# Kernel tuning notes

Measured on AMD Instinct MI355X. Metric: run time of the kernel, lower is better.

The kernel has to match this reference:

```python
import jax, jax.numpy as jnp
import numpy as np

NUM_HEADS = 12
LN_EPS = 1e-5


def _layernorm(x, w, b):
    m = jnp.mean(x, axis=-1, keepdims=True)
    v = jnp.mean(jnp.square(x - m), axis=-1, keepdims=True)
    return (x - m) * jax.lax.rsqrt(v + LN_EPS) * w + b


def setup_inputs() -> dict:
    key = jax.random.key(0)
    ks = jax.random.split(key, 6)
    B, N, C, H = 8, 1024, 768, 3072
    s = 0.02
    return {
        "x": jax.random.normal(ks[0], (B, N, C), jnp.float32),
        "ln1_w": jnp.ones((C,), jnp.float32),
        "ln1_b": jnp.zeros((C,), jnp.float32),
        "qkv_w": jax.random.normal(ks[1], (3 * C, C), jnp.float32) * s,
        "qkv_b": jnp.zeros((3 * C,), jnp.float32),
        "proj_w": jax.random.normal(ks[2], (C, C), jnp.float32) * s,
        "proj_b": jnp.zeros((C,), jnp.float32),
        "ln2_w": jnp.ones((C,), jnp.float32),
        "ln2_b": jnp.zeros((C,), jnp.float32),
        "fc1_w": jax.random.normal(ks[3], (H, C), jnp.float32) * s,
        "fc1_b": jnp.zeros((H,), jnp.float32),
        "fc2_w": jax.random.normal(ks[4], (C, H), jnp.float32) * s,
        "fc2_b": jnp.zeros((C,), jnp.float32),
    }


def reference(x, ln1_w, ln1_b, qkv_w, qkv_b, proj_w, proj_b,
              ln2_w, ln2_b, fc1_w, fc1_b, fc2_w, fc2_b):
    B, N, C = x.shape
    H = NUM_HEADS
    d = C // H
    scale = d ** (-0.5)

    # --- attention on norm1(x) (size=None path, dropout rates are 0) ---
    h = _layernorm(x, ln1_w, ln1_b)
    qkv = h @ qkv_w.T + qkv_b                      # [B,N,3C]
    qkv = qkv.reshape(B, N, 3, H, d).transpose(2, 0, 3, 1, 4)  # [3,B,H,N,d]
    q, k, v = qkv[0], qkv[1], qkv[2]
    attn = jnp.einsum('bhqd,bhkd->bhqk', q, k) * scale
    attn = jax.nn.softmax(attn, axis=-1)
    o = jnp.einsum('bhqk,bhkd->bhqd', attn, v)     # [B,H,N,d]
    o = o.transpose(0, 2, 1, 3).reshape(B, N, C)
    x_attn = o @ proj_w.T + proj_b

    # --- residual + MLP ---
    x = x + x_attn
    h2 = _layernorm(x, ln2_w, ln2_b)
    h2 = jax.nn.gelu(h2 @ fc1_w.T + fc1_b, approximate=False)
    x = x + (h2 @ fc2_w.T + fc2_b)
    return x
```

## Files before the change

### kernel.cpp

```cpp
#include <hip/hip_runtime.h>
#include <cmath>

typedef __bf16 bf16;
typedef __bf16 bf16x8 __attribute__((ext_vector_type(8)));
typedef __bf16 bf16x4 __attribute__((ext_vector_type(4)));
typedef __bf16 bf16x2 __attribute__((ext_vector_type(2)));
typedef float floatx4 __attribute__((ext_vector_type(4)));

#define MFMA16(A, B, C) __builtin_amdgcn_mfma_f32_16x16x32_bf16((A), (B), (C), 0, 0, 0)

#define GLDS16(g, l)                                                   \
  __builtin_amdgcn_global_load_lds(                                    \
      (const __attribute__((address_space(1))) void*)(g),              \
      (__attribute__((address_space(3))) void*)(l), 16, 0, 0)

static __device__ __forceinline__ int pack2(float a, float b) {
  bf16x2 t;
  t[0] = (bf16)a;
  t[1] = (bf16)b;
  return __builtin_bit_cast(int, t);
}

__global__ __launch_bounds__(256) void pre_kernel(
    const float* __restrict__ x, const float* __restrict__ g,
    const float* __restrict__ be, bf16* __restrict__ h1,
    const float* __restrict__ s0, bf16* __restrict__ d0, int n0,
    const float* __restrict__ s1, bf16* __restrict__ d1, int n1,
    const float* __restrict__ s2, bf16* __restrict__ d2, int n2,
    const float* __restrict__ s3, bf16* __restrict__ d3, int n3) {
  int bid = blockIdx.x;
  int t = threadIdx.x;
  if (bid < 8192) {
    const float* xr = x + (size_t)bid * 768;
    float v0 = xr[t], v1 = xr[t + 256], v2 = xr[t + 512];
    float s = v0 + v1 + v2;
    float s2 = v0 * v0 + v1 * v1 + v2 * v2;
#pragma unroll
    for (int o = 1; o < 64; o <<= 1) {
      s += __shfl_xor(s, o, 64);
      s2 += __shfl_xor(s2, o, 64);
    }
    __shared__ float red[8];
    int w = t >> 6, lane = t & 63;
    if (lane == 0) { red[w] = s; red[4 + w] = s2; }
    __syncthreads();
    float ts = red[0] + red[1] + red[2] + red[3];
    float ts2 = red[4] + red[5] + red[6] + red[7];
    float mean = ts * (1.0f / 768.0f);
    float var = ts2 * (1.0f / 768.0f) - mean * mean;
    float rstd = rsqrtf(var + 1e-5f);
    bf16* orow = h1 + (size_t)bid * 768;
    orow[t]       = (bf16)((v0 - mean) * rstd * g[t]       + be[t]);
    orow[t + 256] = (bf16)((v1 - mean) * rstd * g[t + 256] + be[t + 256]);
    orow[t + 512] = (bf16)((v2 - mean) * rstd * g[t + 512] + be[t + 512]);
    return;
  }
  int i = (bid - 8192) * 256 + t;
  const float* s;
  bf16* d;
  if (i < n0) { s = s0 + (size_t)i * 4; d = d0 + (size_t)i * 4; }
  else if ((i -= n0) < n1) { s = s1 + (size_t)i * 4; d = d1 + (size_t)i * 4; }
  else if ((i -= n1) < n2) { s = s2 + (size_t)i * 4; d = d2 + (size_t)i * 4; }
  else if ((i -= n2) < n3) { s = s3 + (size_t)i * 4; d = d3 + (size_t)i * 4; }
  else return;
  bf16x4 v;
  v[0] = (bf16)s[0]; v[1] = (bf16)s[1]; v[2] = (bf16)s[2]; v[3] = (bf16)s[3];
  *(bf16x4*)d = v;
}

__global__ __launch_bounds__(256) void ln_kernel(const float* __restrict__ x,
                                                 const float* __restrict__ g,
                                                 const float* __restrict__ be,
                                                 bf16* __restrict__ out) {
  int row = blockIdx.x;
  int t = threadIdx.x;
  const float* xr = x + (size_t)row * 768;
  float v0 = xr[t], v1 = xr[t + 256], v2 = xr[t + 512];
  float s = v0 + v1 + v2;
  float s2 = v0 * v0 + v1 * v1 + v2 * v2;
#pragma unroll
  for (int o = 1; o < 64; o <<= 1) {
    s += __shfl_xor(s, o, 64);
    s2 += __shfl_xor(s2, o, 64);
  }
  __shared__ float red[8];
  int w = t >> 6, lane = t & 63;
  if (lane == 0) { red[w] = s; red[4 + w] = s2; }
  __syncthreads();
  float ts = red[0] + red[1] + red[2] + red[3];
  float ts2 = red[4] + red[5] + red[6] + red[7];
  float mean = ts * (1.0f / 768.0f);
  float var = ts2 * (1.0f / 768.0f) - mean * mean;
  float rstd = rsqrtf(var + 1e-5f);
  bf16* orow = out + (size_t)row * 768;
  orow[t]       = (bf16)((v0 - mean) * rstd * g[t]       + be[t]);
  orow[t + 256] = (bf16)((v1 - mean) * rstd * g[t + 256] + be[t + 256]);
  orow[t + 512] = (bf16)((v2 - mean) * rstd * g[t + 512] + be[t + 512]);
}

constexpr int EP_BF16 = 0;
constexpr int EP_RES_F32 = 1;
constexpr int EP_GELU_BF16 = 2;

template <int EP, int NJ>
__global__ __launch_bounds__(256, 3) void gemm_bt(
    const bf16* __restrict__ A, const bf16* __restrict__ Bw,
    const float* __restrict__ bias, const float* __restrict__ resid,
    void* __restrict__ outp, int M, int N, int K) {
  __shared__ alignas(16) bf16 Asl[128 * 64];
  __shared__ alignas(16) bf16 Bsl[NJ * 32 * 64];
  int tid = threadIdx.x;
  int lane = tid & 63, w = tid >> 6;
  int wm = w >> 1, wn = w & 1;
  int q16 = lane & 15, quad = lane >> 4;
  int fid = blockIdx.x + gridDim.x * blockIdx.y;
  int nb = gridDim.x;
  int s = fid >> 3;
  int m0 = ((fid & 7) * (gridDim.y >> 3) + s / nb) * 128;
  int n0 = (s % nb) * (NJ * 32);

  floatx4 acc[4][NJ];
#pragma unroll
  for (int i = 0; i < 4; i++)
#pragma unroll
    for (int j = 0; j < NJ; j++) acc[i][j] = (floatx4){0.f, 0.f, 0.f, 0.f};

  int rIn = lane >> 3;
  int cg = (lane & 7) ^ rIn;
  const bf16* ag[4];
  const bf16* bg[NJ];
#pragma unroll
  for (int q = 0; q < 4; q++)
    ag[q] = A + (size_t)(m0 + (w * 4 + q) * 8 + rIn) * K + cg * 8;
#pragma unroll
  for (int q = 0; q < NJ; q++)
    bg[q] = Bw + (size_t)(n0 + (w * NJ + q) * 8 + rIn) * K + cg * 8;
  bf16* la = &Asl[w * 2048];
  bf16* lb = &Bsl[w * NJ * 512];

  int msel = q16 & 7;
  int offA[2][4], offB[2][NJ];
#pragma unroll
  for (int ks = 0; ks < 2; ks++) {
#pragma unroll
    for (int i = 0; i < 4; i++)
      offA[ks][i] = (wm * 64 + i * 16 + q16) * 64 + (((ks * 4 + quad) ^ msel)) * 8;
#pragma unroll
    for (int j = 0; j < NJ; j++)
      offB[ks][j] = (wn * 16 * NJ + j * 16 + q16) * 64 + (((ks * 4 + quad) ^ msel)) * 8;
  }

  for (int k0 = 0; k0 < K; k0 += 64) {
    __syncthreads();
#pragma unroll
    for (int q = 0; q < 4; q++) {
      GLDS16(ag[q], la + q * 512);
      ag[q] += 64;
    }
#pragma unroll
    for (int q = 0; q < NJ; q++) {
      GLDS16(bg[q], lb + q * 512);
      bg[q] += 64;
    }
    __syncthreads();
#pragma unroll
    for (int ks = 0; ks < 2; ks++) {
      bf16x8 af[4], bfr[NJ];
#pragma unroll
      for (int i = 0; i < 4; i++) af[i] = *(const bf16x8*)&Asl[offA[ks][i]];
#pragma unroll
      for (int j = 0; j < NJ; j++) bfr[j] = *(const bf16x8*)&Bsl[offB[ks][j]];
#pragma unroll
      for (int i = 0; i < 4; i++)
#pragma unroll
        for (int j = 0; j < NJ; j++) acc[i][j] = MFMA16(af[i], bfr[j], acc[i][j]);
    }
  }

#pragma unroll
  for (int i = 0; i < 4; i++) {
#pragma unroll
    for (int j = 0; j < NJ; j++) {
#pragma unroll
      for (int r = 0; r < 4; r++) {
        int m = m0 + wm * 64 + i * 16 + quad * 4 + r;
        int n = n0 + wn * 16 * NJ + j * 16 + q16;
        size_t idx = (size_t)m * N + n;
        float v = acc[i][j][r] + bias[n];
        if constexpr (EP == EP_BF16) {
          ((bf16*)outp)[idx] = (bf16)v;
        } else if constexpr (EP == EP_RES_F32) {
          ((float*)outp)[idx] = v + resid[idx];
        } else {
          float u = v * (2.3022083f + 0.1029443f * v * v);
          float e = __builtin_amdgcn_exp2f(-u);
          float gv = v * __builtin_amdgcn_rcpf(1.0f + e);
          ((bf16*)outp)[idx] = (bf16)gv;
        }
      }
    }
  }
}

__global__ __launch_bounds__(256, 3) void attn_kernel(const bf16* __restrict__ qkv,
                                                      bf16* __restrict__ o) {
  __shared__ alignas(16) bf16 Kl[2][64 * 64];
  __shared__ alignas(16) bf16 Vt[2][64 * 72];
  int tid = threadIdx.x;
  int lane = tid & 63, w = tid >> 6;
  int q16 = lane & 15, quad = lane >> 4;
  int b = blockIdx.y / 12, h = blockIdx.y % 12;
  int qbase = blockIdx.x * 128 + w * 32;
  const int KS = 64 * 2304;

  bf16x8 qf[2][2];
#pragma unroll
  for (int qt = 0; qt < 2; qt++)
#pragma unroll
    for (int c = 0; c < 2; c++)
      qf[qt][c] = *(const bf16x8*)(qkv +
          (size_t)(b * 1024 + qbase + qt * 16 + q16) * 2304 + h * 64 +
          c * 32 + quad * 8);

  int krow = lane >> 3;
  int kchunk = (lane & 7) ^ krow;
  const bf16* kg0 = qkv + (size_t)(b * 1024 + w * 16 + krow) * 2304 + 768 +
                    h * 64 + kchunk * 8;
  const bf16* kg1 = kg0 + 8 * 2304;
  bf16* kdA[2] = {&Kl[0][w * 1024], &Kl[1][w * 1024]};

  int kr = tid >> 2;
  int dbase = (tid & 3) * 16;
  const bf16* vgA = qkv + (size_t)(b * 1024 + kr) * 2304 + 1536 + h * 64 + dbase;
  const bf16* vgB = vgA + 8;
  int vtA[8], vtB[8];
#pragma unroll
  for (int e = 0; e < 8; e++) {
    int dA = dbase + e;
    int dB = dbase + 8 + e;
    vtA[e] = ((dA * 9 + (kr >> 3)) ^ ((dA >> 3) & 7)) * 8 + (kr & 7);
    vtB[e] = ((dB * 9 + (kr >> 3)) ^ ((dB >> 3) & 7)) * 8 + (kr & 7);
  }

  int koff[4][2];
#pragma unroll
  for (int nc = 0; nc < 4; nc++)
#pragma unroll
    for (int ck = 0; ck < 2; ck++) {
      int key = nc * 16 + q16;
      koff[nc][ck] = (key * 8 + ((ck * 4 + quad) ^ (key & 7))) * 8;
    }
  int voff[2][4];
#pragma unroll
  for (int c = 0; c < 2; c++)
#pragma unroll
    for (int dc = 0; dc < 4; dc++) {
      int d = dc * 16 + q16;
      voff[c][dc] = ((d * 9 + (c * 4 + quad)) ^ ((d >> 3) & 7)) * 8;
    }

  int srcLo = q16 + ((quad & 1) << 5);
  int srcHi = srcLo + 16;
  bool loH = quad < 2;

  float lsum[2] = {0.f, 0.f};
  floatx4 oacc[2][4];
#pragma unroll
  for (int qt = 0; qt < 2; qt++)
#pragma unroll
    for (int dc = 0; dc < 4; dc++) oacc[qt][dc] = (floatx4){0.f, 0.f, 0.f, 0.f};

  GLDS16(kg0, kdA[0]);
  GLDS16(kg1, kdA[0] + 512);
  kg0 += KS; kg1 += KS;
  bf16x8 va = *(const bf16x8*)vgA;
  bf16x8 vb = *(const bf16x8*)vgB;
  vgA += KS; vgB += KS;
#pragma unroll
  for (int e = 0; e < 8; e++) Vt[0][vtA[e]] = va[e];
#pragma unroll
  for (int e = 0; e < 8; e++) Vt[0][vtB[e]] = vb[e];
  va = *(const bf16x8*)vgA;
  vb = *(const bf16x8*)vgB;
  vgA += KS; vgB += KS;

  for (int kt = 0; kt < 16; kt++) {
    int cur = kt & 1, nxt = cur ^ 1;
    __syncthreads();
    if (kt < 15) {
      GLDS16(kg0, kdA[nxt]);
      GLDS16(kg1, kdA[nxt] + 512);
      kg0 += KS; kg1 += KS;
#pragma unroll
      for (int e = 0; e < 8; e++) Vt[nxt][vtA[e]] = va[e];
#pragma unroll
      for (int e = 0; e < 8; e++) Vt[nxt][vtB[e]] = vb[e];
      if (kt < 14) {
        va = *(const bf16x8*)vgA;
        vb = *(const bf16x8*)vgB;
        vgA += KS; vgB += KS;
      }
    }

    floatx4 z[2][4];
#pragma unroll
    for (int nc = 0; nc < 4; nc++) {
      bf16x8 k0 = *(const bf16x8*)&Kl[cur][koff[nc][0]];
      bf16x8 k1 = *(const bf16x8*)&Kl[cur][koff[nc][1]];
#pragma unroll
      for (int qt = 0; qt < 2; qt++) {
        floatx4 t = (floatx4){0.f, 0.f, 0.f, 0.f};
        t = MFMA16(k0, qf[qt][0], t);
        t = MFMA16(k1, qf[qt][1], t);
        z[qt][nc] = t;
      }
    }

    bf16x8 vf[2][4];
#pragma unroll
    for (int c = 0; c < 2; c++)
#pragma unroll
      for (int dc = 0; dc < 4; dc++)
        vf[c][dc] = *(const bf16x8*)&Vt[cur][voff[c][dc]];

#pragma unroll
    for (int qt = 0; qt < 2; qt++) {
      float e_[4][4];
#pragma unroll
      for (int nc = 0; nc < 4; nc++)
#pragma unroll
        for (int r = 0; r < 4; r++) {
          e_[nc][r] = __builtin_amdgcn_exp2f(z[qt][nc][r] * 0.18033688011f);
          lsum[qt] += e_[nc][r];
        }
      int P[4][2];
#pragma unroll
      for (int nc = 0; nc < 4; nc++) {
        P[nc][0] = pack2(e_[nc][0], e_[nc][1]);
        P[nc][1] = pack2(e_[nc][2], e_[nc][3]);
      }
      union { int i[4]; bf16x8 v; } pu[2];
#pragma unroll
      for (int c = 0; c < 2; c++) {
        int a0 = __shfl(P[2 * c][0], srcLo, 64), b0 = __shfl(P[2 * c + 1][0], srcLo, 64);
        int a1 = __shfl(P[2 * c][1], srcLo, 64), b1 = __shfl(P[2 * c + 1][1], srcLo, 64);
        int a2 = __shfl(P[2 * c][0], srcHi, 64), b2 = __shfl(P[2 * c + 1][0], srcHi, 64);
        int a3 = __shfl(P[2 * c][1], srcHi, 64), b3 = __shfl(P[2 * c + 1][1], srcHi, 64);
        pu[c].i[0] = loH ? a0 : b0;
        pu[c].i[1] = loH ? a1 : b1;
        pu[c].i[2] = loH ? a2 : b2;
        pu[c].i[3] = loH ? a3 : b3;
      }
#pragma unroll
      for (int dc = 0; dc < 4; dc++) {
        oacc[qt][dc] = MFMA16(pu[0].v, vf[0][dc], oacc[qt][dc]);
        oacc[qt][dc] = MFMA16(pu[1].v, vf[1][dc], oacc[qt][dc]);
      }
    }
  }

#pragma unroll
  for (int qt = 0; qt < 2; qt++) {
    float s = lsum[qt];
    s += __shfl_xor(s, 16, 64);
    s += __shfl_xor(s, 32, 64);
    float inv = 1.0f / s;
    bf16* op = o + (size_t)(b * 1024 + qbase + qt * 16) * 768 + h * 64;
#pragma unroll
    for (int r = 0; r < 4; r++) {
      float invr = __shfl(inv, quad * 4 + r, 64);
#pragma unroll
      for (int dc = 0; dc < 4; dc++)
        op[(size_t)(quad * 4 + r) * 768 + dc * 16 + q16] =
            (bf16)(oacc[qt][dc][r] * invr);
    }
  }
}

extern "C" void kernel_launch(void* const* d_in, const int* in_sizes, int n_in,
                              void* d_out, int out_size, void* d_ws, size_t ws_size,
                              hipStream_t stream) {
  (void)in_sizes; (void)n_in; (void)out_size; (void)ws_size;
  const float* x      = (const float*)d_in[0];
  const float* ln1_w  = (const float*)d_in[1];
  const float* ln1_b  = (const float*)d_in[2];
  const float* qkv_w  = (const float*)d_in[3];
  const float* qkv_b  = (const float*)d_in[4];
  const float* proj_w = (const float*)d_in[5];
  const float* proj_b = (const float*)d_in[6];
  const float* ln2_w  = (const float*)d_in[7];
  const float* ln2_b  = (const float*)d_in[8];
  const float* fc1_w  = (const float*)d_in[9];
  const float* fc1_b  = (const float*)d_in[10];
  const float* fc2_w  = (const float*)d_in[11];
  const float* fc2_b  = (const float*)d_in[12];

  char* ws = (char*)d_ws;
  size_t off = 0;
  auto alloc = [&](size_t bytes) {
    void* p = ws + off;
    off += (bytes + 255) & ~(size_t)255;
    return p;
  };
  bf16* wq  = (bf16*)alloc((size_t)2304 * 768 * 2);
  bf16* wp  = (bf16*)alloc((size_t)768 * 768 * 2);
  bf16* wf1 = (bf16*)alloc((size_t)3072 * 768 * 2);
  bf16* wf2 = (bf16*)alloc((size_t)768 * 3072 * 2);
  bf16* slotA = (bf16*)alloc((size_t)8192 * 768 * 2);
  bf16* slotB = (bf16*)alloc((size_t)8192 * 3072 * 2);
  float* x1 = (float*)alloc((size_t)8192 * 768 * 4);

  bf16* h1 = slotA;
  bf16* qkvb = slotB;
  bf16* ob = slotA;
  bf16* h2 = slotA;
  bf16* hm = slotB;

  pre_kernel<<<8192 + 6912, 256, 0, stream>>>(
      x, ln1_w, ln1_b, h1,
      qkv_w, wq, 2304 * 768 / 4, proj_w, wp, 768 * 768 / 4,
      fc1_w, wf1, 3072 * 768 / 4, fc2_w, wf2, 768 * 3072 / 4);

  gemm_bt<EP_BF16, 4><<<dim3(18, 64), 256, 0, stream>>>(
      h1, wq, qkv_b, nullptr, qkvb, 8192, 2304, 768);
  attn_kernel<<<dim3(8, 96), 256, 0, stream>>>(qkvb, ob);
  gemm_bt<EP_RES_F32, 2><<<dim3(12, 64), 256, 0, stream>>>(
      ob, wp, proj_b, x, x1, 8192, 768, 768);
  ln_kernel<<<8192, 256, 0, stream>>>(x1, ln2_w, ln2_b, h2);
  gemm_bt<EP_GELU_BF16, 4><<<dim3(24, 64), 256, 0, stream>>>(
      h2, wf1, fc1_b, nullptr, hm, 8192, 3072, 768);
  gemm_bt<EP_RES_F32, 2><<<dim3(12, 64), 256, 0, stream>>>(
      hm, wf2, fc2_b, x1, (float*)d_out, 8192, 768, 3072);
}
```

Measured before the change: 343.4 us.

## Template GEMM K-tile depth, vectorize V transpose, reorder attention grid

The GEMM kernel now takes a templated K-tile depth BK with a generalized swizzle. The two N=768 projection GEMMs use BK=128, which halves the number of k-loop iterations and barriers at the cost of more shared memory per block. The attention kernel's V transpose into LDS now does 8-byte loads of four rows and packs them with bit shuffles, replacing 16 scalar bf16 LDS stores per thread. The attention grid is swapped so batch-head varies fastest, which changes block scheduling and L2 locality.

```diff
diff --git a/kernel.cpp b/kernel.cpp
--- a/kernel.cpp
+++ b/kernel.cpp
@@ -6,6 +6,7 @@
 typedef __bf16 bf16x4 __attribute__((ext_vector_type(4)));
 typedef __bf16 bf16x2 __attribute__((ext_vector_type(2)));
 typedef float floatx4 __attribute__((ext_vector_type(4)));
+typedef unsigned int uint;
 
 #define MFMA16(A, B, C) __builtin_amdgcn_mfma_f32_16x16x32_bf16((A), (B), (C), 0, 0, 0)
 
@@ -102,13 +103,18 @@
 constexpr int EP_RES_F32 = 1;
 constexpr int EP_GELU_BF16 = 2;
 
-template <int EP, int NJ>
+template <int EP, int NJ, int BK>
 __global__ __launch_bounds__(256, 3) void gemm_bt(
     const bf16* __restrict__ A, const bf16* __restrict__ Bw,
     const float* __restrict__ bias, const float* __restrict__ resid,
     void* __restrict__ outp, int M, int N, int K) {
-  __shared__ alignas(16) bf16 Asl[128 * 64];
-  __shared__ alignas(16) bf16 Bsl[NJ * 32 * 64];
+  constexpr int GR = BK / 8;
+  constexpr int RC = 64 / GR;
+  constexpr int ACH = 128 / RC / 4;
+  constexpr int BCH = (32 * NJ) / RC / 4;
+  constexpr int NKS = BK / 32;
+  __shared__ alignas(16) bf16 Asl[128 * BK];
+  __shared__ alignas(16) bf16 Bsl[NJ * 32 * BK];
   int tid = threadIdx.x;
   int lane = tid & 63, w = tid >> 6;
   int wm = w >> 1, wn = w & 1;
@@ -125,46 +131,50 @@
 #pragma unroll
     for (int j = 0; j < NJ; j++) acc[i][j] = (floatx4){0.f, 0.f, 0.f, 0.f};
 
-  int rIn = lane >> 3;
-  int cg = (lane & 7) ^ rIn;
-  const bf16* ag[4];
-  const bf16* bg[NJ];
-#pragma unroll
-  for (int q = 0; q < 4; q++)
-    ag[q] = A + (size_t)(m0 + (w * 4 + q) * 8 + rIn) * K + cg * 8;
-#pragma unroll
-  for (int q = 0; q < NJ; q++)
-    bg[q] = Bw + (size_t)(n0 + (w * NJ + q) * 8 + rIn) * K + cg * 8;
-  bf16* la = &Asl[w * 2048];
-  bf16* lb = &Bsl[w * NJ * 512];
-
-  int msel = q16 & 7;
-  int offA[2][4], offB[2][NJ];
-#pragma unroll
-  for (int ks = 0; ks < 2; ks++) {
+  int rIn = lane / GR;
+  int sl = lane & (GR - 1);
+  const bf16* ag[ACH];
+  const bf16* bg[BCH];
+#pragma unroll
+  for (int q = 0; q < ACH; q++) {
+    int row = (w * ACH + q) * RC + rIn;
+    ag[q] = A + (size_t)(m0 + row) * K + (size_t)(sl ^ (row & (GR - 1))) * 8;
+  }
+#pragma unroll
+  for (int q = 0; q < BCH; q++) {
+    int row = (w * BCH + q) * RC + rIn;
+    bg[q] = Bw + (size_t)(n0 + row) * K + (size_t)(sl ^ (row & (GR - 1))) * 8;
+  }
+  bf16* la = &Asl[w * ACH * 512];
+  bf16* lb = &Bsl[w * BCH * 512];
+
+  int swz = q16 & (GR - 1);
+  int offA[NKS][4], offB[NKS][NJ];
+#pragma unroll
+  for (int ks = 0; ks < NKS; ks++) {
 #pragma unroll
     for (int i = 0; i < 4; i++)
-      offA[ks][i] = (wm * 64 + i * 16 + q16) * 64 + (((ks * 4 + quad) ^ msel)) * 8;
+      offA[ks][i] = (wm * 64 + i * 16 + q16) * BK + ((ks * 4 + quad) ^ swz) * 8;
 #pragma unroll
     for (int j = 0; j < NJ; j++)
-      offB[ks][j] = (wn * 16 * NJ + j * 16 + q16) * 64 + (((ks * 4 + quad) ^ msel)) * 8;
-  }
-
-  for (int k0 = 0; k0 < K; k0 += 64) {
+      offB[ks][j] = (wn * 16 * NJ + j * 16 + q16) * BK + ((ks * 4 + quad) ^ swz) * 8;
+  }
+
+  for (int k0 = 0; k0 < K; k0 += BK) {
     __syncthreads();
 #pragma unroll
-    for (int q = 0; q < 4; q++) {
+    for (int q = 0; q < ACH; q++) {
       GLDS16(ag[q], la + q * 512);
-      ag[q] += 64;
-    }
-#pragma unroll
-    for (int q = 0; q < NJ; q++) {
+      ag[q] += BK;
+    }
+#pragma unroll
+    for (int q = 0; q < BCH; q++) {
       GLDS16(bg[q], lb + q * 512);
-      bg[q] += 64;
+      bg[q] += BK;
     }
     __syncthreads();
 #pragma unroll
-    for (int ks = 0; ks < 2; ks++) {
+    for (int ks = 0; ks < NKS; ks++) {
       bf16x8 af[4], bfr[NJ];
 #pragma unroll
       for (int i = 0; i < 4; i++) af[i] = *(const bf16x8*)&Asl[offA[ks][i]];
@@ -209,8 +219,8 @@
   int tid = threadIdx.x;
   int lane = tid & 63, w = tid >> 6;
   int q16 = lane & 15, quad = lane >> 4;
-  int b = blockIdx.y / 12, h = blockIdx.y % 12;
-  int qbase = blockIdx.x * 128 + w * 32;
+  int b = blockIdx.x / 12, h = blockIdx.x % 12;
+  int qbase = blockIdx.y * 128 + w * 32;
   const int KS = 64 * 2304;
 
   bf16x8 qf[2][2];
@@ -229,18 +239,17 @@
   const bf16* kg1 = kg0 + 8 * 2304;
   bf16* kdA[2] = {&Kl[0][w * 1024], &Kl[1][w * 1024]};
 
-  int kr = tid >> 2;
-  int dbase = (tid & 3) * 16;
-  const bf16* vgA = qkv + (size_t)(b * 1024 + kr) * 2304 + 1536 + h * 64 + dbase;
-  const bf16* vgB = vgA + 8;
-  int vtA[8], vtB[8];
-#pragma unroll
-  for (int e = 0; e < 8; e++) {
-    int dA = dbase + e;
-    int dB = dbase + 8 + e;
-    vtA[e] = ((dA * 9 + (kr >> 3)) ^ ((dA >> 3) & 7)) * 8 + (kr & 7);
-    vtB[e] = ((dB * 9 + (kr >> 3)) ^ ((dB >> 3) & 7)) * 8 + (kr & 7);
-  }
+  int kg = tid >> 4;
+  int dg = tid & 15;
+  const bf16* vgp = qkv + (size_t)(b * 1024 + 4 * kg) * 2304 + 1536 + h * 64 +
+                    4 * dg;
+  int vw[4];
+#pragma unroll
+  for (int j = 0; j < 4; j++) {
+    int d = 4 * dg + j;
+    vw[j] = (((d * 9 + (kg >> 1)) ^ ((d >> 3) & 7)) * 8) + (kg & 1) * 4;
+  }
+  uint2 vr[4];
 
   int koff[4][2];
 #pragma unroll
@@ -270,19 +279,38 @@
 #pragma unroll
     for (int dc = 0; dc < 4; dc++) oacc[qt][dc] = (floatx4){0.f, 0.f, 0.f, 0.f};
 
+#define VLOAD()                                                        \
+  do {                                                                 \
+    _Pragma("unroll") for (int i = 0; i < 4; i++)                      \
+        vr[i] = *(const uint2*)(vgp + i * 2304);                       \
+    vgp += KS;                                                         \
+  } while (0)
+
+#define VWRITE(buf)                                                    \
+  do {                                                                 \
+    uint lo0 = vr[0].x, lo1 = vr[1].x, lo2 = vr[2].x, lo3 = vr[3].x;   \
+    uint hi0 = vr[0].y, hi1 = vr[1].y, hi2 = vr[2].y, hi3 = vr[3].y;   \
+    uint2 c0, c1, c2, c3;                                              \
+    c0.x = (lo0 & 0xFFFFu) | (lo1 << 16);                              \
+    c0.y = (lo2 & 0xFFFFu) | (lo3 << 16);                              \
+    c1.x = (lo0 >> 16) | (lo1 & 0xFFFF0000u);                          \
+    c1.y = (lo2 >> 16) | (lo3 & 0xFFFF0000u);                          \
+    c2.x = (hi0 & 0xFFFFu) | (hi1 << 16);                              \
+    c2.y = (hi2 & 0xFFFFu) | (hi3 << 16);                              \
+    c3.x = (hi0 >> 16) | (hi1 & 0xFFFF0000u);                          \
+    c3.y = (hi2 >> 16) | (hi3 & 0xFFFF0000u);                          \
+    *(uint2*)&Vt[buf][vw[0]] = c0;                                     \
+    *(uint2*)&Vt[buf][vw[1]] = c1;                                     \
+    *(uint2*)&Vt[buf][vw[2]] = c2;                                     \
+    *(uint2*)&Vt[buf][vw[3]] = c3;                                     \
+  } while (0)
+
   GLDS16(kg0, kdA[0]);
   GLDS16(kg1, kdA[0] + 512);
   kg0 += KS; kg1 += KS;
-  bf16x8 va = *(const bf16x8*)vgA;
-  bf16x8 vb = *(const bf16x8*)vgB;
-  vgA += KS; vgB += KS;
-#pragma unroll
-  for (int e = 0; e < 8; e++) Vt[0][vtA[e]] = va[e];
-#pragma unroll
-  for (int e = 0; e < 8; e++) Vt[0][vtB[e]] = vb[e];
-  va = *(const bf16x8*)vgA;
-  vb = *(const bf16x8*)vgB;
-  vgA += KS; vgB += KS;
+  VLOAD();
+  VWRITE(0);
+  VLOAD();
 
   for (int kt = 0; kt < 16; kt++) {
     int cur = kt & 1, nxt = cur ^ 1;
@@ -291,15 +319,8 @@
       GLDS16(kg0, kdA[nxt]);
       GLDS16(kg1, kdA[nxt] + 512);
       kg0 += KS; kg1 += KS;
-#pragma unroll
-      for (int e = 0; e < 8; e++) Vt[nxt][vtA[e]] = va[e];
-#pragma unroll
-      for (int e = 0; e < 8; e++) Vt[nxt][vtB[e]] = vb[e];
-      if (kt < 14) {
-        va = *(const bf16x8*)vgA;
-        vb = *(const bf16x8*)vgB;
-        vgA += KS; vgB += KS;
-      }
+      VWRITE(nxt);
+      if (kt < 14) VLOAD();
     }
 
     floatx4 z[2][4];
@@ -375,6 +396,8 @@
             (bf16)(oacc[qt][dc][r] * invr);
     }
   }
+#undef VLOAD
+#undef VWRITE
 }
 
 extern "C" void kernel_launch(void* const* d_in, const int* in_sizes, int n_in,
@@ -421,14 +444,14 @@
       qkv_w, wq, 2304 * 768 / 4, proj_w, wp, 768 * 768 / 4,
       fc1_w, wf1, 3072 * 768 / 4, fc2_w, wf2, 768 * 3072 / 4);
 
-  gemm_bt<EP_BF16, 4><<<dim3(18, 64), 256, 0, stream>>>(
+  gemm_bt<EP_BF16, 4, 64><<<dim3(18, 64), 256, 0, stream>>>(
       h1, wq, qkv_b, nullptr, qkvb, 8192, 2304, 768);
-  attn_kernel<<<dim3(8, 96), 256, 0, stream>>>(qkvb, ob);
-  gemm_bt<EP_RES_F32, 2><<<dim3(12, 64), 256, 0, stream>>>(
+  attn_kernel<<<dim3(96, 8), 256, 0, stream>>>(qkvb, ob);
+  gemm_bt<EP_RES_F32, 2, 128><<<dim3(12, 64), 256, 0, stream>>>(
       ob, wp, proj_b, x, x1, 8192, 768, 768);
   ln_kernel<<<8192, 256, 0, stream>>>(x1, ln2_w, ln2_b, h2);
-  gemm_bt<EP_GELU_BF16, 4><<<dim3(24, 64), 256, 0, stream>>>(
+  gemm_bt<EP_GELU_BF16, 4, 64><<<dim3(24, 64), 256, 0, stream>>>(
       h2, wf1, fc1_b, nullptr, hm, 8192, 3072, 768);
-  gemm_bt<EP_RES_F32, 2><<<dim3(12, 64), 256, 0, stream>>>(
+  gemm_bt<EP_RES_F32, 2, 128><<<dim3(12, 64), 256, 0, stream>>>(
       hm, wf2, fc2_b, x1, (float*)d_out, 8192, 768, 3072);
 }
```

New measurement: 326.1 us. 1.05x faster.
